# Kernel optimization log

Hardware: AMD Instinct MI355X
Metric: run time of the kernel (lower is better)

## Reference

```python
import jax, jax.numpy as jnp
import numpy as np

N = 50000          # num nodes
DEG = 16           # constant out-degree -> edges[:,0] sorted, every node present
E = N * DEG
NODE_IN = 128
NODE_OUT = 64
EDGE_IN = 128
EDGE_OUT = 64      # must equal NODE_OUT for the reshape in the original module


def _xavier_uniform(key, shape):
    fan_in, fan_out = shape[0], shape[1]
    a = np.sqrt(6.0 / (fan_in + fan_out)).astype(np.float32)
    return jax.random.uniform(key, shape, jnp.float32, -a, a)


def setup_inputs() -> dict:
    key = jax.random.key(0)
    k1, k2, k3, k4, k5, k6, k7 = jax.random.split(key, 7)
    node_fts = jax.random.normal(k1, (N, NODE_IN), jnp.float32)
    edge_fts = jax.random.normal(k2, (N, EDGE_IN), jnp.float32)
    # sorted sources with constant degree so unique(src).shape[0] == N and
    # the original's repeat(bincount) trick is equivalent to gather-by-src
    src = jnp.repeat(jnp.arange(N, dtype=jnp.int32), DEG)
    dst = jax.random.randint(k3, (E,), 0, N, dtype=jnp.int32)
    edges = jnp.stack([src, dst], axis=1)  # [E, 2]
    W_node = _xavier_uniform(k4, (NODE_IN, NODE_OUT))
    W_edge = _xavier_uniform(k5, (EDGE_IN, EDGE_OUT))
    a_node = _xavier_uniform(k6, (2 * NODE_OUT, 1))
    a_edge = _xavier_uniform(k7, (NODE_OUT + EDGE_OUT, 1))
    return {"node_fts": node_fts, "edge_fts": edge_fts, "edges": edges,
            "W_node": W_node, "W_edge": W_edge,
            "a_node": a_node, "a_edge": a_edge}


def reference(node_fts, edge_fts, edges, W_node, W_edge, a_node, a_edge):
    src = edges[:, 0]
    h_v = node_fts @ W_node            # [N, NODE_OUT]
    e_v = edge_fts @ W_edge            # [N, EDGE_OUT]

    # gather endpoint features -> [E, 2*NODE_OUT] / [E, NODE_OUT+EDGE_OUT]
    h_pair = h_v[edges].reshape(-1, 2 * NODE_OUT)
    e_pair = e_v[edges].reshape(-1, NODE_OUT + EDGE_OUT)

    leaky = lambda x: jnp.where(x > 0, x, 0.2 * x)
    node_att = leaky((h_pair @ a_node)[:, 0])   # [E]
    edge_att = leaky((e_pair @ a_edge)[:, 0])   # [E]

    node_att = jnp.exp(jnp.clip(node_att, -2.0, 2.0))
    edge_att = jnp.exp(jnp.clip(edge_att, -2.0, 2.0))

    node_sum = jax.ops.segment_sum(node_att, src, num_segments=N)
    edge_sum = jax.ops.segment_sum(edge_att, src, num_segments=N)

    node_att_norm = node_att / node_sum[src]
    edge_att_norm = edge_att / edge_sum[src]

    node_att_var = jnp.var(node_att_norm, ddof=1)  # torch.var is unbiased
    edge_att_var = jnp.var(edge_att_norm, ddof=1)

    node_out = jax.ops.segment_sum(h_pair * node_att_norm[:, None], src, num_segments=N)
    edge_out = jax.ops.segment_sum(e_pair * edge_att_norm[:, None], src, num_segments=N)
    return node_out, edge_out, node_att_var, edge_att_var
```

## Files before the change

### kernel.cpp

```cpp
#include <hip/hip_runtime.h>
#include <hip/hip_bf16.h>

#define NN 50000
#define DEG 16
#define EE (NN*DEG)
#define CHUNKS 3125

typedef unsigned int uint;
typedef __attribute__((ext_vector_type(8))) short bf16x8;
typedef __attribute__((ext_vector_type(4))) float f32x4;

__device__ inline unsigned short f2b(float f){
  uint u = __float_as_uint(f);
  uint r = (u + 0x7FFFu + ((u >> 16) & 1u)) >> 16;
  return (unsigned short)r;
}

__global__ __launch_bounds__(256) void gemm_mfma_kernel(
    const float* __restrict__ in0, const float* __restrict__ in1,
    const float* __restrict__ W0,  const float* __restrict__ W1,
    const float* __restrict__ a0,  const float* __restrict__ a1,
    unsigned short* __restrict__ tab0, unsigned short* __restrict__ tab1,
    float* __restrict__ s1ne, float* __restrict__ s2ne,
    float* __restrict__ outp)
{
  const int pass = blockIdx.y;
  const float* in   = pass ? in1 : in0;
  const float* W    = pass ? W1  : W0;
  const float* av   = pass ? a1  : a0;
  unsigned short* tab = pass ? tab1 : tab0;
  float* outhalf = outp + (long)pass * NN * 128;

  __shared__ unsigned short Wt[64*128];
  const int tid = threadIdx.x;
  for (int b = tid; b < 1024; b += 256) {
    const int n  = b >> 4;
    const int k0 = (b & 15) * 8;
    uint4 pk;
    unsigned short* ps = (unsigned short*)&pk;
    #pragma unroll
    for (int j = 0; j < 8; j++) ps[j] = f2b(W[(k0 + j)*64 + n]);
    const int byte = n*256 + ((k0*2) ^ ((n & 7) << 4));
    *(uint4*)((char*)Wt + byte) = pk;
  }
  __syncthreads();

  const int wv   = tid >> 6;
  const int lane = tid & 63;
  const int g    = lane >> 4;
  const int c    = lane & 15;

  bf16x8 wfrag[4][4];
  #pragma unroll
  for (int kt = 0; kt < 4; kt++) {
    #pragma unroll
    for (int nt = 0; nt < 4; nt++) {
      const int n  = nt*16 + c;
      const int kb = (kt*32 + g*8) * 2;
      const int byte = n*256 + (kb ^ ((n & 7) << 4));
      wfrag[kt][nt] = *(bf16x8*)((char*)Wt + byte);
    }
  }
  float a1r[4], a2r[4];
  #pragma unroll
  for (int t = 0; t < 4; t++) { a1r[t] = av[t*16 + c]; a2r[t] = av[64 + t*16 + c]; }

  for (int ch = blockIdx.x*4 + wv; ch < CHUNKS; ch += gridDim.x*4) {
    const int r0 = ch * 16;
    const float* rowp = in + (long)(r0 + c)*128 + g*8;
    float4 ald[8];
    #pragma unroll
    for (int kt = 0; kt < 4; kt++) {
      ald[kt*2]   = *(const float4*)(rowp + kt*32);
      ald[kt*2+1] = *(const float4*)(rowp + kt*32 + 4);
    }
    f32x4 acc[4];
    #pragma unroll
    for (int nt = 0; nt < 4; nt++) acc[nt] = (f32x4){0.f, 0.f, 0.f, 0.f};
    #pragma unroll
    for (int kt = 0; kt < 4; kt++) {
      const float4 u = ald[kt*2], w = ald[kt*2+1];
      bf16x8 af;
      af[0] = (short)f2b(u.x); af[1] = (short)f2b(u.y);
      af[2] = (short)f2b(u.z); af[3] = (short)f2b(u.w);
      af[4] = (short)f2b(w.x); af[5] = (short)f2b(w.y);
      af[6] = (short)f2b(w.z); af[7] = (short)f2b(w.w);
      #pragma unroll
      for (int nt = 0; nt < 4; nt++)
        acc[nt] = __builtin_amdgcn_mfma_f32_16x16x32_bf16(af, wfrag[kt][nt], acc[nt], 0, 0, 0);
    }
    float q1v[4], q2v[4];
    #pragma unroll
    for (int v = 0; v < 4; v++) {
      float t1 = 0.f, t2 = 0.f;
      #pragma unroll
      for (int nt = 0; nt < 4; nt++) {
        t1 = fmaf(acc[nt][v], a1r[nt], t1);
        t2 = fmaf(acc[nt][v], a2r[nt], t2);
      }
      #pragma unroll
      for (int off = 1; off < 16; off <<= 1) {
        t1 += __shfl_xor(t1, off);
        t2 += __shfl_xor(t2, off);
      }
      q1v[v] = t1; q2v[v] = t2;
    }
    if (c < 4) {
      const float sv1 = (c==0) ? q1v[0] : (c==1) ? q1v[1] : (c==2) ? q1v[2] : q1v[3];
      const float sv2 = (c==0) ? q2v[0] : (c==1) ? q2v[1] : (c==2) ? q2v[2] : q2v[3];
      const int r = r0 + g*4 + c;
      s1ne[(long)r*2 + pass] = sv1;
      s2ne[(long)r*2 + pass] = sv2;
    }
    #pragma unroll
    for (int nt = 0; nt < 4; nt++) {
      #pragma unroll
      for (int v = 0; v < 4; v++) {
        const float x = acc[nt][v];
        const long r = r0 + g*4 + v;
        outhalf[r*128 + nt*16 + c] = x;
        tab[r*64 + nt*16 + c]     = f2b(x);
      }
    }
  }
}

__global__ __launch_bounds__(256) void attn_kernel(
    const __hip_bfloat16* __restrict__ hvb, const __hip_bfloat16* __restrict__ evb,
    const float2* __restrict__ s1ne, const float2* __restrict__ s2ne,
    const int* __restrict__ edges,
    float* __restrict__ outp, double* __restrict__ partials)
{
  const int tid  = threadIdx.x;
  const int wv   = tid >> 6;
  const int lane = tid & 63;
  double a_qn = 0.0, a_qe = 0.0;
  float* node_out = outp;
  float* edge_out = outp + (long)NN*128;
  for (int i = blockIdx.x*4 + wv; i < NN; i += gridDim.x*4) {
    const float2 s1v = s1ne[i];
    int dk = 0;
    float attn = 0.f, atte = 0.f;
    if (lane < 16) {
      dk = edges[((long)i*16 + lane)*2 + 1];
      const float2 gsc = s2ne[dk];
      float xn = s1v.x + gsc.x;
      float xe = s1v.y + gsc.y;
      xn = xn > 0.f ? xn : 0.2f*xn;
      xe = xe > 0.f ? xe : 0.2f*xe;
      xn = fminf(fmaxf(xn, -2.f), 2.f);
      xe = fminf(fmaxf(xe, -2.f), 2.f);
      attn = expf(xn);
      atte = expf(xe);
    }
    float sn = attn, se = atte;
    #pragma unroll
    for (int off = 1; off < 16; off <<= 1) {
      sn += __shfl_xor(sn, off);
      se += __shfl_xor(se, off);
    }
    float wn = 0.f, we = 0.f;
    if (lane < 16) { wn = attn / sn; we = atte / se; }
    float rq_n = wn*wn, rq_e = we*we;
    #pragma unroll
    for (int off = 1; off < 16; off <<= 1) {
      rq_n += __shfl_xor(rq_n, off);
      rq_e += __shfl_xor(rq_e, off);
    }
    if (lane == 0) { a_qn += (double)rq_n; a_qe += (double)rq_e; }
    float accn = 0.f, acce = 0.f;
    #pragma unroll
    for (int k = 0; k < 16; k++) {
      const int d     = __shfl(dk, k);
      const float wnk = __shfl(wn, k);
      const float wek = __shfl(we, k);
      accn = fmaf(wnk, __bfloat162float(hvb[(long)d*64 + lane]), accn);
      acce = fmaf(wek, __bfloat162float(evb[(long)d*64 + lane]), acce);
    }
    node_out[(long)i*128 + 64 + lane] = accn;
    edge_out[(long)i*128 + 64 + lane] = acce;
  }
  __shared__ double red[4][2];
  if (lane == 0) { red[wv][0] = a_qn; red[wv][1] = a_qe; }
  __syncthreads();
  if (tid == 0) {
    double t0 = 0, t1 = 0;
    #pragma unroll
    for (int w = 0; w < 4; w++) { t0 += red[w][0]; t1 += red[w][1]; }
    double* p = partials + (long)blockIdx.x*2;
    p[0] = t0; p[1] = t1;
  }
}

__global__ __launch_bounds__(256) void finalize_kernel(
    const double* __restrict__ partials, int nparts, float* __restrict__ outp)
{
  const int tid = threadIdx.x;
  double l0 = 0, l1 = 0;
  for (int b = tid; b < nparts; b += 256) {
    l0 += partials[b*2+0]; l1 += partials[b*2+1];
  }
  __shared__ double red[256][2];
  red[tid][0] = l0; red[tid][1] = l1;
  __syncthreads();
  for (int s = 128; s > 0; s >>= 1) {
    if (tid < s) {
      red[tid][0] += red[tid+s][0];
      red[tid][1] += red[tid+s][1];
    }
    __syncthreads();
  }
  if (tid == 0) {
    const double E = (double)EE;
    const double S = (double)NN;
    double varn = (red[0][0] - S*S/E) / (E - 1.0);
    double vare = (red[0][1] - S*S/E) / (E - 1.0);
    outp[(long)NN*256 + 0] = (float)varn;
    outp[(long)NN*256 + 1] = (float)vare;
  }
}

extern "C" void kernel_launch(void* const* d_in, const int* in_sizes, int n_in,
                              void* d_out, int out_size, void* d_ws, size_t ws_size,
                              hipStream_t stream)
{
  const float* node_fts = (const float*)d_in[0];
  const float* edge_fts = (const float*)d_in[1];
  const int*   edges    = (const int*)d_in[2];
  const float* W_node   = (const float*)d_in[3];
  const float* W_edge   = (const float*)d_in[4];
  const float* a_node   = (const float*)d_in[5];
  const float* a_edge   = (const float*)d_in[6];

  char* ws = (char*)d_ws;
  unsigned short* hvb = (unsigned short*)(ws);
  unsigned short* evb = (unsigned short*)(ws + 6400000);
  float* s1ne = (float*)(ws + 12800000);
  float* s2ne = (float*)(ws + 13200000);
  double* partials = (double*)(ws + 13600000);
  float* outp = (float*)d_out;

  hipLaunchKernelGGL(gemm_mfma_kernel, dim3(391, 2), dim3(256), 0, stream,
                     node_fts, edge_fts, W_node, W_edge, a_node, a_edge,
                     hvb, evb, s1ne, s2ne, outp);
  const int AB = 2048;
  hipLaunchKernelGGL(attn_kernel, dim3(AB), dim3(256), 0, stream,
                     (const __hip_bfloat16*)hvb, (const __hip_bfloat16*)evb,
                     (const float2*)s1ne, (const float2*)s2ne,
                     edges, outp, partials);
  hipLaunchKernelGGL(finalize_kernel, dim3(1), dim3(256), 0, stream,
                     partials, AB, outp);
}
```

Baseline: 77.42 us.

## Interleave node/edge bf16 tables and emit own-feature outputs from attention kernel

The GEMM kernel now writes one interleaved bf16 table of 128 columns per node (node half, then edge half) and no longer writes fp32 outputs. The attention kernel fetches each neighbor's full 256-byte row with one coalesced gather. Lanes 0-31 handle the node half and lanes 32-63 the edge half, and each lane writes whole contiguous output rows as float2, including the self-feature half read back from the table. This removes the separate fp32 output pass and halves the number of gather transactions. The trade-off is that the self-feature output half is now bf16-rounded instead of exact fp32.

```diff
diff --git a/kernel.cpp b/kernel.cpp
--- a/kernel.cpp
+++ b/kernel.cpp
@@ -15,21 +15,19 @@
   uint r = (u + 0x7FFFu + ((u >> 16) & 1u)) >> 16;
   return (unsigned short)r;
 }
+__device__ inline float b2f(uint lo16){ return __uint_as_float(lo16 << 16); }
 
 __global__ __launch_bounds__(256) void gemm_mfma_kernel(
     const float* __restrict__ in0, const float* __restrict__ in1,
     const float* __restrict__ W0,  const float* __restrict__ W1,
     const float* __restrict__ a0,  const float* __restrict__ a1,
-    unsigned short* __restrict__ tab0, unsigned short* __restrict__ tab1,
-    float* __restrict__ s1ne, float* __restrict__ s2ne,
-    float* __restrict__ outp)
+    unsigned short* __restrict__ hev,
+    float* __restrict__ s1ne, float* __restrict__ s2ne)
 {
   const int pass = blockIdx.y;
   const float* in   = pass ? in1 : in0;
   const float* W    = pass ? W1  : W0;
   const float* av   = pass ? a1  : a0;
-  unsigned short* tab = pass ? tab1 : tab0;
-  float* outhalf = outp + (long)pass * NN * 128;
 
   __shared__ unsigned short Wt[64*128];
   const int tid = threadIdx.x;
@@ -116,17 +114,15 @@
     for (int nt = 0; nt < 4; nt++) {
       #pragma unroll
       for (int v = 0; v < 4; v++) {
-        const float x = acc[nt][v];
         const long r = r0 + g*4 + v;
-        outhalf[r*128 + nt*16 + c] = x;
-        tab[r*64 + nt*16 + c]     = f2b(x);
+        hev[r*128 + pass*64 + nt*16 + c] = f2b(acc[nt][v]);
       }
     }
   }
 }
 
 __global__ __launch_bounds__(256) void attn_kernel(
-    const __hip_bfloat16* __restrict__ hvb, const __hip_bfloat16* __restrict__ evb,
+    const uint* __restrict__ hev,
     const float2* __restrict__ s1ne, const float2* __restrict__ s2ne,
     const int* __restrict__ edges,
     float* __restrict__ outp, double* __restrict__ partials)
@@ -134,6 +130,8 @@
   const int tid  = threadIdx.x;
   const int wv   = tid >> 6;
   const int lane = tid & 63;
+  const int cc   = lane & 31;
+  const int sel  = (lane >= 32) ? 16 : 0;
   double a_qn = 0.0, a_qe = 0.0;
   float* node_out = outp;
   float* edge_out = outp + (long)NN*128;
@@ -168,17 +166,22 @@
       rq_e += __shfl_xor(rq_e, off);
     }
     if (lane == 0) { a_qn += (double)rq_n; a_qe += (double)rq_e; }
-    float accn = 0.f, acce = 0.f;
+    const float we_lo = __shfl(we, lane & 15);
+    const float wboth = (lane < 16) ? wn : we_lo;
+    const uint own = hev[(long)i*64 + lane];
+    const float o0 = b2f(own & 0xffffu), o1 = b2f(own >> 16);
+    float acc0 = 0.f, acc1 = 0.f;
     #pragma unroll
     for (int k = 0; k < 16; k++) {
-      const int d     = __shfl(dk, k);
-      const float wnk = __shfl(wn, k);
-      const float wek = __shfl(we, k);
-      accn = fmaf(wnk, __bfloat162float(hvb[(long)d*64 + lane]), accn);
-      acce = fmaf(wek, __bfloat162float(evb[(long)d*64 + lane]), acce);
-    }
-    node_out[(long)i*128 + 64 + lane] = accn;
-    edge_out[(long)i*128 + 64 + lane] = acce;
+      const int d    = __shfl(dk, k);
+      const float wk = __shfl(wboth, sel + k);
+      const uint v   = hev[(long)d*64 + lane];
+      acc0 = fmaf(wk, b2f(v & 0xffffu), acc0);
+      acc1 = fmaf(wk, b2f(v >> 16), acc1);
+    }
+    float* base = (lane < 32 ? node_out : edge_out) + (long)i*128 + 2*cc;
+    *(float2*)(base)      = make_float2(o0, o1);
+    *(float2*)(base + 64) = make_float2(acc0, acc1);
   }
   __shared__ double red[4][2];
   if (lane == 0) { red[wv][0] = a_qn; red[wv][1] = a_qe; }
@@ -233,8 +236,7 @@
   const float* a_edge   = (const float*)d_in[6];
 
   char* ws = (char*)d_ws;
-  unsigned short* hvb = (unsigned short*)(ws);
-  unsigned short* evb = (unsigned short*)(ws + 6400000);
+  unsigned short* hev = (unsigned short*)(ws);
   float* s1ne = (float*)(ws + 12800000);
   float* s2ne = (float*)(ws + 13200000);
   double* partials = (double*)(ws + 13600000);
@@ -242,10 +244,10 @@
 
   hipLaunchKernelGGL(gemm_mfma_kernel, dim3(391, 2), dim3(256), 0, stream,
                      node_fts, edge_fts, W_node, W_edge, a_node, a_edge,
-                     hvb, evb, s1ne, s2ne, outp);
+                     hev, s1ne, s2ne);
   const int AB = 2048;
   hipLaunchKernelGGL(attn_kernel, dim3(AB), dim3(256), 0, stream,
-                     (const __hip_bfloat16*)hvb, (const __hip_bfloat16*)evb,
+                     (const uint*)hev,
                      (const float2*)s1ne, (const float2*)s2ne,
                      edges, outp, partials);
   hipLaunchKernelGGL(finalize_kernel, dim3(1), dim3(256), 0, stream,
```

Result: no change. 78.80 us (+1.8%).
